# Performance work log

Hardware: AMD Instinct MI355X
Metric: run time of the kernel (lower is better)

The kernel has to match this reference:

```python
import jax, jax.numpy as jnp
import numpy as np

LN_EPS = 1e-5


def setup_inputs() -> dict:
    key = jax.random.key(0)
    ks = jax.random.split(key, 8)
    N, E, D = 50000, 800000, 128
    x = jax.random.normal(ks[0], (N, D), dtype=jnp.float32)
    edge_index = jax.random.randint(ks[1], (2, E), 0, N, dtype=jnp.int64)
    scale = 0.05
    return {
        "x": x,
        "edge_index": edge_index,
        "W1": jax.random.normal(ks[2], (2 * D, D), dtype=jnp.float32) * scale,
        "b1": jnp.zeros((D,), dtype=jnp.float32),
        "W2": jax.random.normal(ks[3], (D, D), dtype=jnp.float32) * scale,
        "b2": jnp.zeros((D,), dtype=jnp.float32),
        "W3": jax.random.normal(ks[4], (D, D), dtype=jnp.float32) * scale,
        "b3": jnp.zeros((D,), dtype=jnp.float32),
        "W4": jax.random.normal(ks[5], (D, D), dtype=jnp.float32) * scale,
        "b4": jnp.zeros((D,), dtype=jnp.float32),
        "gamma": jnp.ones((D,), dtype=jnp.float32),
        "beta": jnp.zeros((D,), dtype=jnp.float32),
    }


def _layernorm(h, gamma, beta):
    mu = jnp.mean(h, axis=-1, keepdims=True)
    var = jnp.mean(jnp.square(h - mu), axis=-1, keepdims=True)
    return (h - mu) * jax.lax.rsqrt(var + LN_EPS) * gamma + beta


def reference(x, edge_index, W1, b1, W2, b2, W3, b3, W4, b4, gamma, beta):
    num_nodes = x.shape[0]
    senders, receivers = edge_index[0], edge_index[1]
    # gather sender features [E, D], scatter-add to receivers -> [N, D]
    agg = jax.ops.segment_sum(x[senders], receivers, num_segments=num_nodes)
    h = jnp.concatenate([x, agg], axis=-1)  # [N, 2D]
    h = jax.nn.relu(h @ W1 + b1)
    h = jax.nn.relu(h @ W2 + b2)
    h = jax.nn.relu(h @ W3 + b3)
    h = h @ W4 + b4
    return _layernorm(h, gamma, beta)
```

## Files before the change

### kernel.cpp

```cpp
#include <hip/hip_runtime.h>
#include <hip/hip_bf16.h>

typedef short short8 __attribute__((ext_vector_type(8)));
typedef float f32x4 __attribute__((ext_vector_type(4)));

#define LN_EPS 1e-5f
#define NBLK 256

__device__ __forceinline__ unsigned short f2bf(float f) {
    unsigned int u = __builtin_bit_cast(unsigned int, f);
    unsigned int r = (u + 0x7FFFu + ((u >> 16) & 1u)) >> 16;
    return (unsigned short)r;
}
__device__ __forceinline__ float bf_lo(unsigned int v) {
    return __builtin_bit_cast(float, v << 16);
}
__device__ __forceinline__ float bf_hi(unsigned int v) {
    return __builtin_bit_cast(float, v & 0xFFFF0000u);
}

__device__ __forceinline__ bool edges_are_i64(const int* ei) {
    return ((ei[1] | ei[3] | ei[5] | ei[7]) == 0);
}

__global__ __launch_bounds__(256) void prep_kernel(
    const float* __restrict__ W1, const float* __restrict__ W2,
    const float* __restrict__ W3, const float* __restrict__ W4,
    unsigned short* __restrict__ wt1, unsigned short* __restrict__ wt2,
    unsigned short* __restrict__ wt3, unsigned short* __restrict__ wt4)
{
    int idx = blockIdx.x * 256 + threadIdx.x;
    if (idx < 32768) {
        int k = idx >> 7, n = idx & 127;
        wt1[n * 256 + k] = f2bf(W1[idx]);
    } else if (idx < 49152) {
        int j = idx - 32768; int k = j >> 7, n = j & 127;
        wt2[n * 128 + k] = f2bf(W2[j]);
    } else if (idx < 65536) {
        int j = idx - 49152; int k = j >> 7, n = j & 127;
        wt3[n * 128 + k] = f2bf(W3[j]);
    } else if (idx < 81920) {
        int j = idx - 65536; int k = j >> 7, n = j & 127;
        wt4[n * 128 + k] = f2bf(W4[j]);
    }
}

__global__ __launch_bounds__(256) void xcvt_kernel(
    const float4* __restrict__ x4, uint4* __restrict__ xb4, int total8)
{
    int i = blockIdx.x * 256 + threadIdx.x;
    if (i >= total8) return;
    float4 a = x4[i * 2], b = x4[i * 2 + 1];
    uint4 o;
    o.x = (unsigned int)f2bf(a.x) | ((unsigned int)f2bf(a.y) << 16);
    o.y = (unsigned int)f2bf(a.z) | ((unsigned int)f2bf(a.w) << 16);
    o.z = (unsigned int)f2bf(b.x) | ((unsigned int)f2bf(b.y) << 16);
    o.w = (unsigned int)f2bf(b.z) | ((unsigned int)f2bf(b.w) << 16);
    xb4[i] = o;
}

__global__ __launch_bounds__(256) void bucket_hist_kernel(
    const int* __restrict__ ei, int* __restrict__ BBC, int E, int chunk)
{
    __shared__ int hist[256];
    int t = threadIdx.x, blk = blockIdx.x;
    hist[t] = 0;
    __syncthreads();
    int beg = blk * chunk;
    int end = min(E, beg + chunk);
    if (edges_are_i64(ei)) {
        const long long* e64 = (const long long*)ei;
        for (int e = beg + t; e < end; e += 256)
            atomicAdd(&hist[((int)e64[E + e]) >> 8], 1);
    } else {
        for (int e = beg + t; e < end; e += 256)
            atomicAdd(&hist[ei[E + e] >> 8], 1);
    }
    __syncthreads();
    BBC[t * NBLK + blk] = hist[t];
}

__global__ __launch_bounds__(256) void bucket_scan1_kernel(
    const int* __restrict__ BBC, int* __restrict__ BBL, int* __restrict__ bucketTotal)
{
    __shared__ int sd[256];
    int t = threadIdx.x, b = blockIdx.x;
    int v = BBC[b * NBLK + t];
    sd[t] = v;
    __syncthreads();
    for (int d = 1; d < 256; d <<= 1) {
        int add = (t >= d) ? sd[t - d] : 0;
        __syncthreads();
        sd[t] += add;
        __syncthreads();
    }
    BBL[b * NBLK + t] = sd[t] - v;
    if (t == 255) bucketTotal[b] = sd[255];
}

__global__ __launch_bounds__(256) void bucket_scan2_kernel(
    const int* __restrict__ bucketTotal, int* __restrict__ bucketBase)
{
    __shared__ int sd[256];
    int t = threadIdx.x;
    int v = bucketTotal[t];
    sd[t] = v;
    __syncthreads();
    for (int d = 1; d < 256; d <<= 1) {
        int add = (t >= d) ? sd[t - d] : 0;
        __syncthreads();
        sd[t] += add;
        __syncthreads();
    }
    bucketBase[t] = sd[t] - v;
    if (t == 255) bucketBase[256] = sd[255];
}

__global__ __launch_bounds__(256) void bucket_scatter_kernel(
    const int* __restrict__ ei, const int* __restrict__ BBL,
    const int* __restrict__ bucketBase, unsigned int* __restrict__ packed,
    int E, int chunk)
{
    __shared__ int cur[256];
    int t = threadIdx.x, blk = blockIdx.x;
    cur[t] = bucketBase[t] + BBL[t * NBLK + blk];
    __syncthreads();
    int beg = blk * chunk;
    int end = min(E, beg + chunk);
    if (edges_are_i64(ei)) {
        const long long* e64 = (const long long*)ei;
        for (int e = beg + t; e < end; e += 256) {
            int s = (int)e64[e], r = (int)e64[E + e];
            int pos = atomicAdd(&cur[r >> 8], 1);
            packed[pos] = (unsigned int)s | ((unsigned int)(r & 255) << 24);
        }
    } else {
        for (int e = beg + t; e < end; e += 256) {
            int s = ei[e], r = ei[E + e];
            int pos = atomicAdd(&cur[r >> 8], 1);
            packed[pos] = (unsigned int)s | ((unsigned int)(r & 255) << 24);
        }
    }
}

__global__ __launch_bounds__(256) void bucket_sort_kernel(
    const unsigned int* __restrict__ packed, const int* __restrict__ bucketBase,
    int* __restrict__ offsets, int* __restrict__ sorted, int N)
{
    __shared__ int hist[256];
    __shared__ int sd[256];
    int t = threadIdx.x, b = blockIdx.x;
    int beg = bucketBase[b], end = bucketBase[b + 1];
    hist[t] = 0;
    __syncthreads();
    for (int i = beg + t; i < end; i += 256)
        atomicAdd(&hist[packed[i] >> 24], 1);
    __syncthreads();
    int v = hist[t];
    sd[t] = v;
    __syncthreads();
    for (int d = 1; d < 256; d <<= 1) {
        int add = (t >= d) ? sd[t - d] : 0;
        __syncthreads();
        sd[t] += add;
        __syncthreads();
    }
    int excl = sd[t] - v;
    int idx = b * 256 + t;
    if (idx <= N) offsets[idx] = beg + excl;
    hist[t] = excl;
    __syncthreads();
    for (int i = beg + t; i < end; i += 256) {
        unsigned int p = packed[i];
        int rl = (int)(p >> 24);
        int pos = beg + atomicAdd(&hist[rl], 1);
        sorted[pos] = (int)(p & 0xFFFFFFu);
    }
}

template<bool BF>
__global__ __launch_bounds__(256) void aggregate_kernel(
    const void* __restrict__ xsrc, const int* __restrict__ offsets,
    const int* __restrict__ sorted, float2* __restrict__ agg2, int N)
{
    int wave = threadIdx.x >> 6, lane = threadIdx.x & 63;
    int r = blockIdx.x * 4 + wave;
    if (r >= N) return;
    int beg = offsets[r], end = offsets[r + 1];
    const unsigned int* xb = (const unsigned int*)xsrc;
    const float2* x2 = (const float2*)xsrc;
    float ax0 = 0, ay0 = 0, ax1 = 0, ay1 = 0;
    float ax2 = 0, ay2 = 0, ax3 = 0, ay3 = 0;
    int i = beg;
    for (; i + 4 <= end; i += 4) {
        int s0 = sorted[i + 0];
        int s1 = sorted[i + 1];
        int s2 = sorted[i + 2];
        int s3 = sorted[i + 3];
        if constexpr (BF) {
            unsigned int v0 = xb[(size_t)s0 * 64 + lane];
            unsigned int v1 = xb[(size_t)s1 * 64 + lane];
            unsigned int v2 = xb[(size_t)s2 * 64 + lane];
            unsigned int v3 = xb[(size_t)s3 * 64 + lane];
            ax0 += bf_lo(v0); ay0 += bf_hi(v0);
            ax1 += bf_lo(v1); ay1 += bf_hi(v1);
            ax2 += bf_lo(v2); ay2 += bf_hi(v2);
            ax3 += bf_lo(v3); ay3 += bf_hi(v3);
        } else {
            float2 v0 = x2[(size_t)s0 * 64 + lane];
            float2 v1 = x2[(size_t)s1 * 64 + lane];
            float2 v2 = x2[(size_t)s2 * 64 + lane];
            float2 v3 = x2[(size_t)s3 * 64 + lane];
            ax0 += v0.x; ay0 += v0.y;
            ax1 += v1.x; ay1 += v1.y;
            ax2 += v2.x; ay2 += v2.y;
            ax3 += v3.x; ay3 += v3.y;
        }
    }
    for (; i < end; ++i) {
        int s = sorted[i];
        if constexpr (BF) {
            unsigned int v = xb[(size_t)s * 64 + lane];
            ax0 += bf_lo(v); ay0 += bf_hi(v);
        } else {
            float2 v = x2[(size_t)s * 64 + lane];
            ax0 += v.x; ay0 += v.y;
        }
    }
    float2 o;
    o.x = (ax0 + ax1) + (ax2 + ax3);
    o.y = (ay0 + ay1) + (ay2 + ay3);
    agg2[(size_t)r * 64 + lane] = o;
}

template<int K, bool RELU>
__device__ __forceinline__ void layer_bf16(
    const unsigned short* Hin, int sin,
    const unsigned short* __restrict__ Wt, const float* __restrict__ bias,
    unsigned short* Hout, int sout, int tid)
{
    int lane = tid & 63;
    int w = tid >> 6;
    int r0 = lane & 15, quad = lane >> 4;
    int col0 = w * 32 + r0;
    int col1 = w * 32 + 16 + r0;
    float bias0 = bias[col0], bias1 = bias[col1];
    f32x4 acc[4][2];
#pragma unroll
    for (int rt = 0; rt < 4; ++rt) { acc[rt][0] = 0.f; acc[rt][1] = 0.f; }
    const unsigned short* wrow0 = Wt + col0 * K + quad * 8;
    const unsigned short* wrow1 = Wt + col1 * K + quad * 8;
    const unsigned short* arow = Hin + r0 * sin + quad * 8;
#pragma unroll
    for (int ks = 0; ks < K / 32; ++ks) {
        short8 bf0 = *(const short8*)(wrow0 + ks * 32);
        short8 bf1 = *(const short8*)(wrow1 + ks * 32);
#pragma unroll
        for (int rt = 0; rt < 4; ++rt) {
            short8 af = *(const short8*)(arow + rt * 16 * sin + ks * 32);
            acc[rt][0] = __builtin_amdgcn_mfma_f32_16x16x32_bf16(af, bf0, acc[rt][0], 0, 0, 0);
            acc[rt][1] = __builtin_amdgcn_mfma_f32_16x16x32_bf16(af, bf1, acc[rt][1], 0, 0, 0);
        }
    }
#pragma unroll
    for (int rt = 0; rt < 4; ++rt) {
#pragma unroll
        for (int i = 0; i < 4; ++i) {
            int row = rt * 16 + quad * 4 + i;
            float v0 = acc[rt][0][i] + bias0;
            float v1 = acc[rt][1][i] + bias1;
            if (RELU) { v0 = fmaxf(v0, 0.f); v1 = fmaxf(v1, 0.f); }
            Hout[row * sout + col0] = f2bf(v0);
            Hout[row * sout + col1] = f2bf(v1);
        }
    }
}

__device__ __forceinline__ void layer_f32out(
    const unsigned short* Hin, int sin,
    const unsigned short* __restrict__ Wt, const float* __restrict__ bias,
    float* Hout, int sout, int tid)
{
    constexpr int K = 128;
    int lane = tid & 63;
    int w = tid >> 6;
    int r0 = lane & 15, quad = lane >> 4;
    int col0 = w * 32 + r0;
    int col1 = w * 32 + 16 + r0;
    float bias0 = bias[col0], bias1 = bias[col1];
    f32x4 acc[4][2];
#pragma unroll
    for (int rt = 0; rt < 4; ++rt) { acc[rt][0] = 0.f; acc[rt][1] = 0.f; }
    const unsigned short* wrow0 = Wt + col0 * K + quad * 8;
    const unsigned short* wrow1 = Wt + col1 * K + quad * 8;
    const unsigned short* arow = Hin + r0 * sin + quad * 8;
#pragma unroll
    for (int ks = 0; ks < K / 32; ++ks) {
        short8 bf0 = *(const short8*)(wrow0 + ks * 32);
        short8 bf1 = *(const short8*)(wrow1 + ks * 32);
#pragma unroll
        for (int rt = 0; rt < 4; ++rt) {
            short8 af = *(const short8*)(arow + rt * 16 * sin + ks * 32);
            acc[rt][0] = __builtin_amdgcn_mfma_f32_16x16x32_bf16(af, bf0, acc[rt][0], 0, 0, 0);
            acc[rt][1] = __builtin_amdgcn_mfma_f32_16x16x32_bf16(af, bf1, acc[rt][1], 0, 0, 0);
        }
    }
#pragma unroll
    for (int rt = 0; rt < 4; ++rt) {
#pragma unroll
        for (int i = 0; i < 4; ++i) {
            int row = rt * 16 + quad * 4 + i;
            Hout[row * sout + col0] = acc[rt][0][i] + bias0;
            Hout[row * sout + col1] = acc[rt][1][i] + bias1;
        }
    }
}

__global__ __launch_bounds__(256) void mlp_kernel(
    const float4* __restrict__ x4, const uint2* __restrict__ xb2, int hasxb,
    const float4* agg4,
    const unsigned short* __restrict__ wt1, const unsigned short* __restrict__ wt2,
    const unsigned short* __restrict__ wt3, const unsigned short* __restrict__ wt4,
    const float* __restrict__ b1, const float* __restrict__ b2,
    const float* __restrict__ b3, const float* __restrict__ b4,
    const float* __restrict__ gamma, const float* __restrict__ beta,
    float4* out4, int N)
{
    __shared__ unsigned char smem[33792 + 17408];
    unsigned short* HA = (unsigned short*)smem;
    unsigned short* HB = (unsigned short*)(smem + 33792);
    float* H4 = (float*)smem;

    int tid = threadIdx.x;
    int node0 = blockIdx.x * 64;

#pragma unroll
    for (int j = 0; j < 8; ++j) {
        int idx = tid + j * 256;
        int row = idx >> 5, c4 = idx & 31;
        int node = node0 + row;
        unsigned short* p = HA + row * 264 + c4 * 4;
        if (hasxb) {
            uint2 vx = make_uint2(0u, 0u);
            if (node < N) vx = xb2[(size_t)node * 32 + c4];
            *(uint2*)p = vx;
        } else {
            float4 vx = make_float4(0.f, 0.f, 0.f, 0.f);
            if (node < N) vx = x4[node * 32 + c4];
            p[0] = f2bf(vx.x); p[1] = f2bf(vx.y); p[2] = f2bf(vx.z); p[3] = f2bf(vx.w);
        }
        float4 va = make_float4(0.f, 0.f, 0.f, 0.f);
        if (node < N) va = agg4[node * 32 + c4];
        unsigned short* q = p + 128;
        q[0] = f2bf(va.x); q[1] = f2bf(va.y); q[2] = f2bf(va.z); q[3] = f2bf(va.w);
    }
    __syncthreads();

    layer_bf16<256, true>(HA, 264, wt1, b1, HB, 136, tid);
    __syncthreads();
    layer_bf16<128, true>(HB, 136, wt2, b2, HA, 136, tid);
    __syncthreads();
    layer_bf16<128, true>(HA, 136, wt3, b3, HB, 136, tid);
    __syncthreads();
    layer_f32out(HB, 136, wt4, b4, H4, 132, tid);
    __syncthreads();

    int row = tid >> 2;
    int part = tid & 3;
    const float* hr = H4 + row * 132 + part * 32;
    float s = 0.f, s2 = 0.f;
#pragma unroll
    for (int j = 0; j < 8; ++j) {
        float4 v = *(const float4*)(hr + j * 4);
        s  += v.x + v.y + v.z + v.w;
        s2 += v.x * v.x + v.y * v.y + v.z * v.z + v.w * v.w;
    }
    s  += __shfl_xor(s, 1);  s  += __shfl_xor(s, 2);
    s2 += __shfl_xor(s2, 1); s2 += __shfl_xor(s2, 2);
    float mu = s * (1.f / 128.f);
    float var = s2 * (1.f / 128.f) - mu * mu;
    float rstd = rsqrtf(fmaxf(var, 0.f) + LN_EPS);
    int node = node0 + row;
    if (node < N) {
#pragma unroll
        for (int j = 0; j < 8; ++j) {
            int c = part * 32 + j * 4;
            float4 v = *(const float4*)(hr + j * 4);
            float4 o;
            o.x = (v.x - mu) * rstd * gamma[c + 0] + beta[c + 0];
            o.y = (v.y - mu) * rstd * gamma[c + 1] + beta[c + 1];
            o.z = (v.z - mu) * rstd * gamma[c + 2] + beta[c + 2];
            o.w = (v.w - mu) * rstd * gamma[c + 3] + beta[c + 3];
            out4[node * 32 + part * 8 + j] = o;
        }
    }
}

extern "C" void kernel_launch(void* const* d_in, const int* in_sizes, int n_in,
                              void* d_out, int out_size, void* d_ws, size_t ws_size,
                              hipStream_t stream) {
    const float* x     = (const float*)d_in[0];
    const int*   edges = (const int*)d_in[1];
    const float* W1 = (const float*)d_in[2];
    const float* b1 = (const float*)d_in[3];
    const float* W2 = (const float*)d_in[4];
    const float* b2 = (const float*)d_in[5];
    const float* W3 = (const float*)d_in[6];
    const float* b3 = (const float*)d_in[7];
    const float* W4 = (const float*)d_in[8];
    const float* b4 = (const float*)d_in[9];
    const float* gamma = (const float*)d_in[10];
    const float* beta  = (const float*)d_in[11];

    int N = in_sizes[0] / 128;
    int E = in_sizes[1] / 2;

    float* agg = (float*)d_out;

    unsigned char* ws = (unsigned char*)d_ws;
    unsigned short* wt1 = (unsigned short*)ws;
    unsigned short* wt2 = wt1 + 128 * 256;
    unsigned short* wt3 = wt2 + 128 * 128;
    unsigned short* wt4 = wt3 + 128 * 128;
    size_t off = (size_t)(128 * 256 + 3 * 128 * 128) * 2;

    size_t packed_bytes = (size_t)E * 4;
    size_t xb_bytes = (size_t)N * 128 * 2;
    size_t region_big = xb_bytes > packed_bytes ? xb_bytes : packed_bytes;
    size_t tail = (size_t)E * 4
                + (size_t)(N + 1) * 4
                + (size_t)2 * 256 * NBLK * 4
                + 256 * 4
                + 260 * 4;
    bool hasxb = ws_size >= off + region_big + tail + 1024;
    size_t region = hasxb ? region_big : packed_bytes;

    unsigned char* p = ws + off;
    unsigned int* packed = (unsigned int*)p;
    unsigned short* xb = (unsigned short*)p;
    p += region;
    int* sorted = (int*)p;      p += (size_t)E * 4;
    int* offsets = (int*)p;     p += (size_t)(N + 1) * 4;
    int* BBC = (int*)p;         p += (size_t)256 * NBLK * 4;
    int* BBL = (int*)p;         p += (size_t)256 * NBLK * 4;
    int* bucketTotal = (int*)p; p += 256 * 4;
    int* bucketBase = (int*)p;

    int chunk = (E + NBLK - 1) / NBLK;

    prep_kernel<<<320, 256, 0, stream>>>(W1, W2, W3, W4, wt1, wt2, wt3, wt4);

    bucket_hist_kernel<<<NBLK, 256, 0, stream>>>(edges, BBC, E, chunk);
    bucket_scan1_kernel<<<256, 256, 0, stream>>>(BBC, BBL, bucketTotal);
    bucket_scan2_kernel<<<1, 256, 0, stream>>>(bucketTotal, bucketBase);
    bucket_scatter_kernel<<<NBLK, 256, 0, stream>>>(edges, BBL, bucketBase, packed, E, chunk);
    bucket_sort_kernel<<<256, 256, 0, stream>>>(packed, bucketBase, offsets, sorted, N);

    if (hasxb) {
        int total8 = N * 16;
        xcvt_kernel<<<(total8 + 255) / 256, 256, 0, stream>>>(
            (const float4*)x, (uint4*)xb, total8);
    }

    int agg_blocks = (N + 3) / 4;
    if (hasxb)
        aggregate_kernel<true><<<agg_blocks, 256, 0, stream>>>(
            (const void*)xb, offsets, sorted, (float2*)agg, N);
    else
        aggregate_kernel<false><<<agg_blocks, 256, 0, stream>>>(
            (const void*)x, offsets, sorted, (float2*)agg, N);

    int mlp_blocks = (N + 63) / 64;
    mlp_kernel<<<mlp_blocks, 256, 0, stream>>>(
        (const float4*)x, (const uint2*)(hasxb ? (const void*)xb : (const void*)nullptr),
        hasxb ? 1 : 0,
        (const float4*)agg,
        wt1, wt2, wt3, wt4, b1, b2, b3, b4, gamma, beta,
        (float4*)d_out, N);
}
```

Baseline: 217.9 us.

## Fuse neighbor aggregation into MLP kernel and merge x conversion into prep

Moves the per-node gather-sum of sender features into the MLP kernel, writing bf16 aggregates directly into shared memory instead of storing an fp32 agg buffer to global memory and reloading it. Also folds the x-to-bf16 conversion into the weight prep kernel, launched after sorting, removing two launches. The trade-off is far fewer waves performing the latency-bound gather, each handling 16 rows serially with occupancy limited by the MLP's shared memory footprint.

```diff
diff --git a/kernel.cpp b/kernel.cpp
--- a/kernel.cpp
+++ b/kernel.cpp
@@ -27,7 +27,8 @@
     const float* __restrict__ W1, const float* __restrict__ W2,
     const float* __restrict__ W3, const float* __restrict__ W4,
     unsigned short* __restrict__ wt1, unsigned short* __restrict__ wt2,
-    unsigned short* __restrict__ wt3, unsigned short* __restrict__ wt4)
+    unsigned short* __restrict__ wt3, unsigned short* __restrict__ wt4,
+    const float4* __restrict__ x4, uint4* __restrict__ xb4, int total8)
 {
     int idx = blockIdx.x * 256 + threadIdx.x;
     if (idx < 32768) {
@@ -42,21 +43,18 @@
     } else if (idx < 81920) {
         int j = idx - 65536; int k = j >> 7, n = j & 127;
         wt4[n * 128 + k] = f2bf(W4[j]);
-    }
-}
-
-__global__ __launch_bounds__(256) void xcvt_kernel(
-    const float4* __restrict__ x4, uint4* __restrict__ xb4, int total8)
-{
-    int i = blockIdx.x * 256 + threadIdx.x;
-    if (i >= total8) return;
-    float4 a = x4[i * 2], b = x4[i * 2 + 1];
-    uint4 o;
-    o.x = (unsigned int)f2bf(a.x) | ((unsigned int)f2bf(a.y) << 16);
-    o.y = (unsigned int)f2bf(a.z) | ((unsigned int)f2bf(a.w) << 16);
-    o.z = (unsigned int)f2bf(b.x) | ((unsigned int)f2bf(b.y) << 16);
-    o.w = (unsigned int)f2bf(b.z) | ((unsigned int)f2bf(b.w) << 16);
-    xb4[i] = o;
+    } else {
+        int i = idx - 81920;
+        if (i < total8) {
+            float4 a = x4[i * 2], b = x4[i * 2 + 1];
+            uint4 o;
+            o.x = (unsigned int)f2bf(a.x) | ((unsigned int)f2bf(a.y) << 16);
+            o.y = (unsigned int)f2bf(a.z) | ((unsigned int)f2bf(a.w) << 16);
+            o.z = (unsigned int)f2bf(b.x) | ((unsigned int)f2bf(b.y) << 16);
+            o.w = (unsigned int)f2bf(b.z) | ((unsigned int)f2bf(b.w) << 16);
+            xb4[i] = o;
+        }
+    }
 }
 
 __global__ __launch_bounds__(256) void bucket_hist_kernel(
@@ -178,61 +176,6 @@
     }
 }
 
-template<bool BF>
-__global__ __launch_bounds__(256) void aggregate_kernel(
-    const void* __restrict__ xsrc, const int* __restrict__ offsets,
-    const int* __restrict__ sorted, float2* __restrict__ agg2, int N)
-{
-    int wave = threadIdx.x >> 6, lane = threadIdx.x & 63;
-    int r = blockIdx.x * 4 + wave;
-    if (r >= N) return;
-    int beg = offsets[r], end = offsets[r + 1];
-    const unsigned int* xb = (const unsigned int*)xsrc;
-    const float2* x2 = (const float2*)xsrc;
-    float ax0 = 0, ay0 = 0, ax1 = 0, ay1 = 0;
-    float ax2 = 0, ay2 = 0, ax3 = 0, ay3 = 0;
-    int i = beg;
-    for (; i + 4 <= end; i += 4) {
-        int s0 = sorted[i + 0];
-        int s1 = sorted[i + 1];
-        int s2 = sorted[i + 2];
-        int s3 = sorted[i + 3];
-        if constexpr (BF) {
-            unsigned int v0 = xb[(size_t)s0 * 64 + lane];
-            unsigned int v1 = xb[(size_t)s1 * 64 + lane];
-            unsigned int v2 = xb[(size_t)s2 * 64 + lane];
-            unsigned int v3 = xb[(size_t)s3 * 64 + lane];
-            ax0 += bf_lo(v0); ay0 += bf_hi(v0);
-            ax1 += bf_lo(v1); ay1 += bf_hi(v1);
-            ax2 += bf_lo(v2); ay2 += bf_hi(v2);
-            ax3 += bf_lo(v3); ay3 += bf_hi(v3);
-        } else {
-            float2 v0 = x2[(size_t)s0 * 64 + lane];
-            float2 v1 = x2[(size_t)s1 * 64 + lane];
-            float2 v2 = x2[(size_t)s2 * 64 + lane];
-            float2 v3 = x2[(size_t)s3 * 64 + lane];
-            ax0 += v0.x; ay0 += v0.y;
-            ax1 += v1.x; ay1 += v1.y;
-            ax2 += v2.x; ay2 += v2.y;
-            ax3 += v3.x; ay3 += v3.y;
-        }
-    }
-    for (; i < end; ++i) {
-        int s = sorted[i];
-        if constexpr (BF) {
-            unsigned int v = xb[(size_t)s * 64 + lane];
-            ax0 += bf_lo(v); ay0 += bf_hi(v);
-        } else {
-            float2 v = x2[(size_t)s * 64 + lane];
-            ax0 += v.x; ay0 += v.y;
-        }
-    }
-    float2 o;
-    o.x = (ax0 + ax1) + (ax2 + ax3);
-    o.y = (ay0 + ay1) + (ay2 + ay3);
-    agg2[(size_t)r * 64 + lane] = o;
-}
-
 template<int K, bool RELU>
 __device__ __forceinline__ void layer_bf16(
     const unsigned short* Hin, int sin,
@@ -316,9 +259,10 @@
     }
 }
 
+template<bool BF>
 __global__ __launch_bounds__(256) void mlp_kernel(
-    const float4* __restrict__ x4, const uint2* __restrict__ xb2, int hasxb,
-    const float4* agg4,
+    const void* __restrict__ xsrc,
+    const int* __restrict__ offsets, const int* __restrict__ sorted,
     const unsigned short* __restrict__ wt1, const unsigned short* __restrict__ wt2,
     const unsigned short* __restrict__ wt3, const unsigned short* __restrict__ wt4,
     const float* __restrict__ b1, const float* __restrict__ b2,
@@ -333,6 +277,8 @@
 
     int tid = threadIdx.x;
     int node0 = blockIdx.x * 64;
+    const unsigned int* xb = (const unsigned int*)xsrc;
+    const float2* x2 = (const float2*)xsrc;
 
 #pragma unroll
     for (int j = 0; j < 8; ++j) {
@@ -340,19 +286,68 @@
         int row = idx >> 5, c4 = idx & 31;
         int node = node0 + row;
         unsigned short* p = HA + row * 264 + c4 * 4;
-        if (hasxb) {
+        if constexpr (BF) {
             uint2 vx = make_uint2(0u, 0u);
-            if (node < N) vx = xb2[(size_t)node * 32 + c4];
+            if (node < N) vx = ((const uint2*)xsrc)[(size_t)node * 32 + c4];
             *(uint2*)p = vx;
         } else {
             float4 vx = make_float4(0.f, 0.f, 0.f, 0.f);
-            if (node < N) vx = x4[node * 32 + c4];
+            if (node < N) vx = ((const float4*)xsrc)[(size_t)node * 32 + c4];
             p[0] = f2bf(vx.x); p[1] = f2bf(vx.y); p[2] = f2bf(vx.z); p[3] = f2bf(vx.w);
         }
-        float4 va = make_float4(0.f, 0.f, 0.f, 0.f);
-        if (node < N) va = agg4[node * 32 + c4];
-        unsigned short* q = p + 128;
-        q[0] = f2bf(va.x); q[1] = f2bf(va.y); q[2] = f2bf(va.z); q[3] = f2bf(va.w);
+    }
+
+    {
+        int wave = tid >> 6, lane = tid & 63;
+        for (int i = 0; i < 16; ++i) {
+            int row = wave * 16 + i;
+            int node = node0 + row;
+            float ax0 = 0, ay0 = 0, ax1 = 0, ay1 = 0;
+            float ax2 = 0, ay2 = 0, ax3 = 0, ay3 = 0;
+            if (node < N) {
+                int beg = offsets[node], end = offsets[node + 1];
+                int e = beg;
+                for (; e + 4 <= end; e += 4) {
+                    int s0 = sorted[e + 0];
+                    int s1 = sorted[e + 1];
+                    int s2 = sorted[e + 2];
+                    int s3 = sorted[e + 3];
+                    if constexpr (BF) {
+                        unsigned int v0 = xb[(size_t)s0 * 64 + lane];
+                        unsigned int v1 = xb[(size_t)s1 * 64 + lane];
+                        unsigned int v2 = xb[(size_t)s2 * 64 + lane];
+                        unsigned int v3 = xb[(size_t)s3 * 64 + lane];
+                        ax0 += bf_lo(v0); ay0 += bf_hi(v0);
+                        ax1 += bf_lo(v1); ay1 += bf_hi(v1);
+                        ax2 += bf_lo(v2); ay2 += bf_hi(v2);
+                        ax3 += bf_lo(v3); ay3 += bf_hi(v3);
+                    } else {
+                        float2 v0 = x2[(size_t)s0 * 64 + lane];
+                        float2 v1 = x2[(size_t)s1 * 64 + lane];
+                        float2 v2 = x2[(size_t)s2 * 64 + lane];
+                        float2 v3 = x2[(size_t)s3 * 64 + lane];
+                        ax0 += v0.x; ay0 += v0.y;
+                        ax1 += v1.x; ay1 += v1.y;
+                        ax2 += v2.x; ay2 += v2.y;
+                        ax3 += v3.x; ay3 += v3.y;
+                    }
+                }
+                for (; e < end; ++e) {
+                    int s = sorted[e];
+                    if constexpr (BF) {
+                        unsigned int v = xb[(size_t)s * 64 + lane];
+                        ax0 += bf_lo(v); ay0 += bf_hi(v);
+                    } else {
+                        float2 v = x2[(size_t)s * 64 + lane];
+                        ax0 += v.x; ay0 += v.y;
+                    }
+                }
+            }
+            float sx = (ax0 + ax1) + (ax2 + ax3);
+            float sy = (ay0 + ay1) + (ay2 + ay3);
+            unsigned int pk = (unsigned int)f2bf(sx) | ((unsigned int)f2bf(sy) << 16);
+            *(unsigned int*)(HA + row * 264 + 128 + 2 * lane) = pk;
+        }
     }
     __syncthreads();
 
@@ -415,8 +410,6 @@
     int N = in_sizes[0] / 128;
     int E = in_sizes[1] / 2;
 
-    float* agg = (float*)d_out;
-
     unsigned char* ws = (unsigned char*)d_ws;
     unsigned short* wt1 = (unsigned short*)ws;
     unsigned short* wt2 = wt1 + 128 * 256;
@@ -448,33 +441,27 @@
 
     int chunk = (E + NBLK - 1) / NBLK;
 
-    prep_kernel<<<320, 256, 0, stream>>>(W1, W2, W3, W4, wt1, wt2, wt3, wt4);
-
     bucket_hist_kernel<<<NBLK, 256, 0, stream>>>(edges, BBC, E, chunk);
     bucket_scan1_kernel<<<256, 256, 0, stream>>>(BBC, BBL, bucketTotal);
     bucket_scan2_kernel<<<1, 256, 0, stream>>>(bucketTotal, bucketBase);
     bucket_scatter_kernel<<<NBLK, 256, 0, stream>>>(edges, BBL, bucketBase, packed, E, chunk);
     bucket_sort_kernel<<<256, 256, 0, stream>>>(packed, bucketBase, offsets, sorted, N);
 
-    if (hasxb) {
-        int total8 = N * 16;
-        xcvt_kernel<<<(total8 + 255) / 256, 256, 0, stream>>>(
-            (const float4*)x, (uint4*)xb, total8);
-    }
-
-    int agg_blocks = (N + 3) / 4;
+    int total8 = hasxb ? N * 16 : 0;
+    int prep_threads = 81920 + total8;
+    prep_kernel<<<(prep_threads + 255) / 256, 256, 0, stream>>>(
+        W1, W2, W3, W4, wt1, wt2, wt3, wt4,
+        (const float4*)x, (uint4*)xb, total8);
+
+    int mlp_blocks = (N + 63) / 64;
     if (hasxb)
-        aggregate_kernel<true><<<agg_blocks, 256, 0, stream>>>(
-            (const void*)xb, offsets, sorted, (float2*)agg, N);
+        mlp_kernel<true><<<mlp_blocks, 256, 0, stream>>>(
+            (const void*)xb, offsets, sorted,
+            wt1, wt2, wt3, wt4, b1, b2, b3, b4, gamma, beta,
+            (float4*)d_out, N);
     else
-        aggregate_kernel<false><<<agg_blocks, 256, 0, stream>>>(
-            (const void*)x, offsets, sorted, (float2*)agg, N);
-
-    int mlp_blocks = (N + 63) / 64;
-    mlp_kernel<<<mlp_blocks, 256, 0, stream>>>(
-        (const float4*)x, (const uint2*)(hasxb ? (const void*)xb : (const void*)nullptr),
-        hasxb ? 1 : 0,
-        (const float4*)agg,
-        wt1, wt2, wt3, wt4, b1, b2, b3, b4, gamma, beta,
-        (float4*)d_out, N);
-}
+        mlp_kernel<false><<<mlp_blocks, 256, 0, stream>>>(
+            (const void*)x, offsets, sorted,
+            wt1, wt2, wt3, wt4, b1, b2, b3, b4, gamma, beta,
+            (float4*)d_out, N);
+}
```

Result: slower. 269.6 us (+23.7%).
